# Kernel tuning notes

Hardware: AMD Instinct MI355X
Metric: run time of the kernel (lower is better)

## Reference

```python
import jax, jax.numpy as jnp
from jax import lax
import numpy as np

B, C, H, W = 2, 128, 64, 64
E = 3            # num_experts
DSTATE = 64      # d_state
DCONV = 4        # d_conv
DIN = 2 * C      # d_inner (expand=2)
DTR = 8          # dt_rank = ceil(C/16)
CONVDIM = 64     # router hidden channels


def mamba_block(xseq, in_w, conv_w, conv_b, xproj_w, dt_w, dt_b, A_log, D, out_w):
    # xseq: (B, L, C)
    Bn, L, _ = xseq.shape
    xr = xseq @ in_w.T                      # (B, L, 2*DIN)
    x, res = jnp.split(xr, 2, axis=-1)
    # depthwise causal conv over sequence dim
    xt = x.transpose(0, 2, 1)               # (B, DIN, L)
    xt = lax.conv_general_dilated(xt, conv_w, window_strides=(1,),
                                  padding=[(DCONV - 1, 0)],
                                  feature_group_count=DIN,
                                  dimension_numbers=('NCW', 'OIW', 'NCW'))
    xt = xt + conv_b[None, :, None]
    x = jax.nn.silu(xt.transpose(0, 2, 1))  # (B, L, DIN)
    # input-dependent SSM params
    dbl = x @ xproj_w.T                     # (B, L, DTR + 2*DSTATE)
    dt, Bm, Cm = dbl[..., :DTR], dbl[..., DTR:DTR + DSTATE], dbl[..., DTR + DSTATE:]
    delta = jax.nn.softplus(dt @ dt_w.T + dt_b)  # (B, L, DIN)
    A = -jnp.exp(A_log)                     # (DIN, DSTATE)

    def step(h, inp):
        d_t, B_t, C_t, u_t = inp            # (B,DIN),(B,DSTATE),(B,DSTATE),(B,DIN)
        dA = jnp.exp(d_t[..., None] * A)    # (B, DIN, DSTATE)
        h = dA * h + (d_t * u_t)[..., None] * B_t[:, None, :]
        y = jnp.einsum('bdn,bn->bd', h, C_t)
        return h, y

    h0 = jnp.zeros((Bn, DIN, DSTATE), x.dtype)
    xs = (delta.transpose(1, 0, 2), Bm.transpose(1, 0, 2),
          Cm.transpose(1, 0, 2), x.transpose(1, 0, 2))
    _, ys = lax.scan(step, h0, xs)          # ys: (L, B, DIN)
    y = ys.transpose(1, 0, 2) + x * D       # skip connection
    y = y * jax.nn.silu(res)                # gate
    return y @ out_w.T                      # (B, L, C)


def setup_inputs() -> dict:
    key = jax.random.key(0)
    ks = jax.random.split(key, 10)
    s = 0.02
    n = lambda k, sh: jax.random.normal(k, sh, jnp.float32) * s
    A_log = jnp.log(jnp.broadcast_to(jnp.arange(1, DSTATE + 1, dtype=jnp.float32),
                                     (E, DIN, DSTATE))) + 0.0
    return {
        'x': jax.random.normal(ks[0], (B, C, H, W), jnp.float32),
        'expert_in_w': n(ks[1], (E, 2 * DIN, C)),
        'expert_conv_w': n(ks[2], (E, DIN, 1, DCONV)),
        'expert_conv_b': jnp.zeros((E, DIN), jnp.float32),
        'expert_xproj_w': n(ks[3], (E, DTR + 2 * DSTATE, DIN)),
        'expert_dt_w': n(ks[4], (E, DIN, DTR)),
        'expert_dt_b': jnp.zeros((E, DIN), jnp.float32),
        'expert_A_log': A_log,
        'expert_D': jnp.ones((E, DIN), jnp.float32),
        'expert_out_w': n(ks[5], (E, C, DIN)),
        'router_conv_w': n(ks[6], (CONVDIM, C, 3, 3)),
        'router_conv_b': jnp.zeros((CONVDIM,), jnp.float32),
        'router_lin_w': n(ks[7], (E, CONVDIM)),
        'router_lin_b': jnp.zeros((E,), jnp.float32),
        'fusion_w': n(ks[8], (C, C)),
        'fusion_b': jnp.zeros((C,), jnp.float32),
    }


def reference(x, expert_in_w, expert_conv_w, expert_conv_b, expert_xproj_w,
              expert_dt_w, expert_dt_b, expert_A_log, expert_D, expert_out_w,
              router_conv_w, router_conv_b, router_lin_w, router_lin_b,
              fusion_w, fusion_b):
    Bn, Cn, Hn, Wn = x.shape
    xseq = x.reshape(Bn, Cn, Hn * Wn).transpose(0, 2, 1)  # (B, L, C)
    # router: conv3x3 -> relu -> global avg pool -> linear -> softmax
    r = lax.conv_general_dilated(x, router_conv_w, (1, 1), 'SAME',
                                 dimension_numbers=('NCHW', 'OIHW', 'NCHW'))
    r = jax.nn.relu(r + router_conv_b[None, :, None, None])
    pooled = r.mean(axis=(2, 3))                          # (B, CONVDIM)
    weights = jax.nn.softmax(pooled @ router_lin_w.T + router_lin_b, axis=1)  # (B, E)
    # run all experts via vmap over the expert axis
    outs = jax.vmap(mamba_block, in_axes=(None, 0, 0, 0, 0, 0, 0, 0, 0, 0))(
        xseq, expert_in_w, expert_conv_w, expert_conv_b, expert_xproj_w,
        expert_dt_w, expert_dt_b, expert_A_log, expert_D, expert_out_w)  # (E,B,L,C)
    outs = outs.transpose(0, 1, 3, 2).reshape(outs.shape[0], Bn, Cn, Hn, Wn)
    ws = jnp.einsum('ebchw,be->bchw', outs, weights)
    out = jnp.einsum('bchw,oc->bohw', ws, fusion_w) + fusion_b[None, :, None, None]
    return out
```

## Files before the change

kernel.cpp:

```cpp
#include <hip/hip_runtime.h>
#include <math.h>
#include <stdint.h>

#define LSEQ 4096
#define NCHUNK 8
#define TC 512

#define AS1 __attribute__((address_space(1)))
#define AS3 __attribute__((address_space(3)))
__device__ __forceinline__ void gload_lds16(const void* g, void* l) {
  __builtin_amdgcn_global_load_lds((const AS1 unsigned int*)g,
                                   (AS3 unsigned int*)l, 16, 0, 0);
}

__global__ __launch_bounds__(256) void k_router_conv(
    const float* __restrict__ x, const float* __restrict__ rcw,
    const float* __restrict__ rcb, float* __restrict__ rpool) {
  int bid = blockIdx.x;
  int ocq = bid & 3;
  int h = (bid >> 2) & 63;
  int b = bid >> 8;
  __shared__ float xs[16][3][66];
  __shared__ float wl[16][145];
  int tid = threadIdx.x;
  int ocl = tid & 15;
  int oc = ocq * 16 + ocl;
  int w0 = (tid >> 4) * 4;
  if (tid < 96) {
    int ic = tid / 6, rr = tid % 6;
    int row = rr >> 1, edge = (rr & 1) ? 65 : 0;
    xs[ic][row][edge] = 0.f;
  }
  float acc[4] = {};
  for (int cc = 0; cc < 8; ++cc) {
    __syncthreads();
#pragma unroll
    for (int i = 0; i < 12; ++i) {
      int f = tid + i * 256;
      int ic = f / 192, rem = f % 192;
      int row = rem / 64, w = rem & 63;
      int hh = h - 1 + row;
      float v = 0.f;
      if (hh >= 0 && hh < 64)
        v = x[((size_t)(b * 128 + cc * 16 + ic) * 64 + hh) * 64 + w];
      xs[ic][row][w + 1] = v;
    }
    for (int f = tid; f < 2304; f += 256) {
      int o = f / 144, r = f % 144;
      wl[o][r] = rcw[(size_t)(ocq * 16 + o) * 1152 + cc * 144 + r];
    }
    __syncthreads();
    for (int ic = 0; ic < 16; ++ic) {
#pragma unroll
      for (int kh = 0; kh < 3; ++kh) {
        float xv[6];
#pragma unroll
        for (int j = 0; j < 6; ++j) xv[j] = xs[ic][kh][w0 + j];
        float w_0 = wl[ocl][ic * 9 + kh * 3 + 0];
        float w_1 = wl[ocl][ic * 9 + kh * 3 + 1];
        float w_2 = wl[ocl][ic * 9 + kh * 3 + 2];
#pragma unroll
        for (int i = 0; i < 4; ++i)
          acc[i] += w_0 * xv[i] + w_1 * xv[i + 1] + w_2 * xv[i + 2];
      }
    }
  }
  float cbv = rcb[oc];
  float t = 0.f;
#pragma unroll
  for (int i = 0; i < 4; ++i) t += fmaxf(acc[i] + cbv, 0.f);
  t += __shfl_xor(t, 16);
  t += __shfl_xor(t, 32);
  if ((tid & 63) < 16) atomicAdd(rpool + b * 64 + oc, t);
}

__global__ __launch_bounds__(64) void k_router_softmax(
    const float* __restrict__ rpool, const float* __restrict__ rlw,
    const float* __restrict__ rlb, float* __restrict__ rw) {
  int t = threadIdx.x;
  __shared__ float logits[2][3];
  for (int b = 0; b < 2; ++b) {
    float p = rpool[b * 64 + t] * (1.0f / 4096.0f);
    for (int e = 0; e < 3; ++e) {
      float v = p * rlw[e * 64 + t];
      for (int off = 32; off; off >>= 1) v += __shfl_xor(v, off);
      if (t == 0) logits[b][e] = v + rlb[e];
    }
  }
  __syncthreads();
  if (t == 0) {
    for (int b = 0; b < 2; ++b) {
      float m = fmaxf(fmaxf(logits[b][0], logits[b][1]), logits[b][2]);
      float e0 = expf(logits[b][0] - m), e1 = expf(logits[b][1] - m),
            e2 = expf(logits[b][2] - m);
      float s = e0 + e1 + e2;
      rw[b * 3 + 0] = e0 / s;
      rw[b * 3 + 1] = e1 / s;
      rw[b * 3 + 2] = e2 / s;
    }
  }
}

__global__ __launch_bounds__(256) void k_wfuse(
    const float* __restrict__ fw, const float* __restrict__ outw,
    float* __restrict__ wf) {
  int e = blockIdx.x >> 7;
  int co = blockIdx.x & 127;
  int k = threadIdx.x;
  float acc = 0.f;
  const float* fwr = fw + (size_t)co * 128;
  const float* ob = outw + (size_t)e * 128 * 256 + k;
#pragma unroll 8
  for (int m = 0; m < 128; ++m) acc = fmaf(fwr[m], ob[(size_t)m * 256], acc);
  wf[((size_t)e * 128 + co) * 256 + k] = acc;
}

__global__ __launch_bounds__(256) void k_gemm_in(
    const float* __restrict__ x, const float* __restrict__ inw,
    float* __restrict__ xr) {
  int eb = blockIdx.y;
  int e = eb >> 1, b = eb & 1;
  int lt = blockIdx.x >> 3;
  int jt = blockIdx.x & 7;
  int l0 = lt * 128, j0 = jt * 64;
  __shared__ float xt[16][128];
  __shared__ float wt[16][64];
  int tid = threadIdx.x;
  int jj = (tid & 15) * 4;
  int lr = (tid >> 4) * 8;
  float acc[8][4] = {};
  const float* xb = x + (size_t)b * 128 * 4096;
  const float* wb = inw + (size_t)e * 512 * 128;
  for (int c0 = 0; c0 < 128; c0 += 16) {
    __syncthreads();
#pragma unroll
    for (int i = 0; i < 2; ++i) {
      int f = tid + i * 256;
      int c = f >> 5;
      int lp = (f & 31) * 4;
      float4 v = *(const float4*)(xb + (size_t)(c0 + c) * 4096 + l0 + lp);
      *(float4*)(&xt[c][lp]) = v;
    }
    {
      int j = tid >> 2;
      int kk = (tid & 3) * 4;
      float4 v = *(const float4*)(wb + (size_t)(j0 + j) * 128 + c0 + kk);
      wt[kk + 0][j] = v.x; wt[kk + 1][j] = v.y;
      wt[kk + 2][j] = v.z; wt[kk + 3][j] = v.w;
    }
    __syncthreads();
#pragma unroll
    for (int k = 0; k < 16; ++k) {
      float4 bv = *(const float4*)(&wt[k][jj]);
      float4 a0 = *(const float4*)(&xt[k][lr]);
      float4 a1 = *(const float4*)(&xt[k][lr + 4]);
      float av[8] = {a0.x, a0.y, a0.z, a0.w, a1.x, a1.y, a1.z, a1.w};
#pragma unroll
      for (int i = 0; i < 8; ++i) {
        acc[i][0] = fmaf(av[i], bv.x, acc[i][0]);
        acc[i][1] = fmaf(av[i], bv.y, acc[i][1]);
        acc[i][2] = fmaf(av[i], bv.z, acc[i][2]);
        acc[i][3] = fmaf(av[i], bv.w, acc[i][3]);
      }
    }
  }
  float* out = xr + (size_t)eb * 4096 * 512;
#pragma unroll
  for (int i = 0; i < 8; ++i) {
    float4 v = {acc[i][0], acc[i][1], acc[i][2], acc[i][3]};
    *(float4*)(out + (size_t)(l0 + lr + i) * 512 + j0 + jj) = v;
  }
}

__global__ __launch_bounds__(256) void k_conv1d(
    const float* __restrict__ xr, const float* __restrict__ cw,
    const float* __restrict__ cb, float* __restrict__ xact) {
  int eb = blockIdx.y;
  int e = eb >> 1;
  int l0 = blockIdx.x * 64;
  int d = threadIdx.x;
  const float* w = cw + (size_t)(e * 256 + d) * 4;
  float w0_ = w[0], w1_ = w[1], w2_ = w[2], w3_ = w[3];
  float bias = cb[e * 256 + d];
  const float* xin = xr + (size_t)eb * 4096 * 512 + d;
  float* xo = xact + (size_t)eb * 4096 * 256 + d;
  float xm3 = (l0 >= 3) ? xin[(size_t)(l0 - 3) * 512] : 0.f;
  float xm2 = (l0 >= 2) ? xin[(size_t)(l0 - 2) * 512] : 0.f;
  float xm1 = (l0 >= 1) ? xin[(size_t)(l0 - 1) * 512] : 0.f;
  for (int i = 0; i < 64; ++i) {
    float xc = xin[(size_t)(l0 + i) * 512];
    float v = bias + w0_ * xm3 + w1_ * xm2 + w2_ * xm1 + w3_ * xc;
    xo[(size_t)(l0 + i) * 256] = v / (1.0f + expf(-v));
    xm3 = xm2; xm2 = xm1; xm1 = xc;
  }
}

__global__ __launch_bounds__(256) void k_gemm_xproj(
    const float* __restrict__ xact, const float* __restrict__ xpw,
    float* __restrict__ dbl) {
  int eb = blockIdx.y;
  int e = eb >> 1;
  int lt = blockIdx.x / 3, jt = blockIdx.x % 3;
  int l0 = lt * 128, j0 = jt * 64;
  __shared__ float at[16][128];
  __shared__ float wt[16][64];
  int tid = threadIdx.x;
  int jj = (tid & 15) * 4;
  int lr = (tid >> 4) * 8;
  float acc[8][4] = {};
  const float* ab = xact + (size_t)eb * 4096 * 256;
  const float* wb = xpw + (size_t)e * 136 * 256;
  for (int k0 = 0; k0 < 256; k0 += 16) {
    __syncthreads();
#pragma unroll
    for (int i = 0; i < 2; ++i) {
      int f = tid + i * 256;
      int l = f >> 2, kq = (f & 3) * 4;
      float4 v = *(const float4*)(ab + (size_t)(l0 + l) * 256 + k0 + kq);
      at[kq + 0][l] = v.x; at[kq + 1][l] = v.y;
      at[kq + 2][l] = v.z; at[kq + 3][l] = v.w;
    }
    {
      int j = tid >> 2, kk = (tid & 3) * 4;
      float4 v = {0, 0, 0, 0};
      if (j0 + j < 136)
        v = *(const float4*)(wb + (size_t)(j0 + j) * 256 + k0 + kk);
      wt[kk + 0][j] = v.x; wt[kk + 1][j] = v.y;
      wt[kk + 2][j] = v.z; wt[kk + 3][j] = v.w;
    }
    __syncthreads();
#pragma unroll
    for (int k = 0; k < 16; ++k) {
      float4 bv = *(const float4*)(&wt[k][jj]);
      float4 a0 = *(const float4*)(&at[k][lr]);
      float4 a1 = *(const float4*)(&at[k][lr + 4]);
      float av[8] = {a0.x, a0.y, a0.z, a0.w, a1.x, a1.y, a1.z, a1.w};
#pragma unroll
      for (int i = 0; i < 8; ++i) {
        acc[i][0] = fmaf(av[i], bv.x, acc[i][0]);
        acc[i][1] = fmaf(av[i], bv.y, acc[i][1]);
        acc[i][2] = fmaf(av[i], bv.z, acc[i][2]);
        acc[i][3] = fmaf(av[i], bv.w, acc[i][3]);
      }
    }
  }
  float* ob = dbl + (size_t)eb * 4096 * 136;
  for (int i = 0; i < 8; ++i)
    for (int q = 0; q < 4; ++q) {
      int j = j0 + jj + q;
      if (j < 136) ob[(size_t)(l0 + lr + i) * 136 + j] = acc[i][q];
    }
}

__global__ __launch_bounds__(256) void k_delta(
    const float* __restrict__ dbl, const float* __restrict__ dtw,
    const float* __restrict__ dtb, const float* __restrict__ xact,
    float* __restrict__ dd) {
  int eb = blockIdx.y;
  int e = eb >> 1;
  int t0 = blockIdx.x * 64;
  int d = threadIdx.x;
  __shared__ float dt8[64][8];
  {
    int f = threadIdx.x;
    for (int i = 0; i < 2; ++i, f += 256) {
      int l = f >> 3, r = f & 7;
      dt8[l][r] = dbl[(size_t)eb * 4096 * 136 + (size_t)(t0 + l) * 136 + r];
    }
  }
  __syncthreads();
  float w[8];
#pragma unroll
  for (int r = 0; r < 8; ++r) w[r] = dtw[(size_t)(e * 256 + d) * 8 + r];
  float bias = dtb[e * 256 + d];
  const float* xa = xact + (size_t)eb * 4096 * 256 + d;
  float4* out = (float4*)dd + (size_t)(eb * 256 + d) * 2048 + (t0 >> 1);
  for (int i = 0; i < 64; i += 2) {
    float v0 = bias, v1 = bias;
#pragma unroll
    for (int r = 0; r < 8; ++r) {
      v0 += dt8[i][r] * w[r];
      v1 += dt8[i + 1][r] * w[r];
    }
    float de0 = fmaxf(v0, 0.f) + log1pf(expf(-fabsf(v0)));
    float de1 = fmaxf(v1, 0.f) + log1pf(expf(-fabsf(v1)));
    float u0 = xa[(size_t)(t0 + i) * 256];
    float u1 = xa[(size_t)(t0 + i + 1) * 256];
    float4 o = {de0, de0 * u0, de1, de1 * u1};
    out[i >> 1] = o;
  }
}

__global__ __launch_bounds__(256) void k_scan1(
    const float* __restrict__ dbl, const float* __restrict__ dd,
    const float* __restrict__ alog, float* __restrict__ prd,
    float* __restrict__ hend) {
  __shared__ float sB[2][16][64];
  int eb = blockIdx.y;
  int e = eb >> 1;
  int c = blockIdx.x >> 6;
  int dgrp = blockIdx.x & 63;
  int wid = threadIdx.x >> 6, lane = threadIdx.x & 63;
  int d = dgrp * 4 + wid;
  float An = -__expf(alog[((size_t)e * 256 + d) * 64 + lane]);
  const float2* ddp = (const float2*)dd + ((size_t)eb * 256 + d) * 4096;
  {
    uint64_t a = (uint64_t)ddp;
    uint32_t lo = __builtin_amdgcn_readfirstlane((int)(uint32_t)a);
    uint32_t hi = __builtin_amdgcn_readfirstlane((int)(uint32_t)(a >> 32));
    ddp = (const float2*)(((uint64_t)hi << 32) | (uint64_t)lo);
  }
  const float* dblb = dbl + (size_t)eb * 4096 * 136;
  int t0 = c * TC;
  int srow = 4 * wid + (lane >> 4);
  int scol = (lane & 15) * 4;
  float h = 0.f, sdel = 0.f;
  gload_lds16(dblb + (size_t)(t0 + srow) * 136 + 8 + scol, &sB[0][4 * wid][0]);
  __syncthreads();
  for (int s = 0; s < 32; ++s) {
    int cur = s & 1;
    int t0s = t0 + s * 16;
    if (s + 1 < 32)
      gload_lds16(dblb + (size_t)(t0s + 16 + srow) * 136 + 8 + scol,
                  &sB[cur ^ 1][4 * wid][0]);
    float2 rdv[16];
#pragma unroll
    for (int j = 0; j < 16; ++j) rdv[j] = ddp[t0s + j];
#pragma unroll
    for (int j = 0; j < 16; ++j) {
      float Bn = sB[cur][j][lane];
      h = fmaf(__expf(rdv[j].x * An), h, rdv[j].y * Bn);
      sdel += rdv[j].x;
    }
    __syncthreads();
  }
  size_t o = (((size_t)eb * 256 + d) * NCHUNK + c) * 64 + lane;
  prd[o] = __expf(An * sdel);
  hend[o] = h;
}

__global__ __launch_bounds__(256) void k_scan2(
    const float* __restrict__ prd, const float* __restrict__ hend,
    float* __restrict__ hinit) {
  int w = blockIdx.x * 4 + (threadIdx.x >> 6);
  int lane = threadIdx.x & 63;
  size_t base = (size_t)w * NCHUNK * 64 + lane;
  float h = 0.f;
  hinit[base] = 0.f;
#pragma unroll
  for (int c = 1; c < NCHUNK; ++c) {
    h = fmaf(prd[base + (c - 1) * 64], h, hend[base + (c - 1) * 64]);
    hinit[base + c * 64] = h;
  }
}

__global__ __launch_bounds__(256) void k_scan3(
    const float* __restrict__ dbl, const float* __restrict__ dd,
    const float* __restrict__ alog, const float* __restrict__ hinit,
    float* __restrict__ ytr) {
  __shared__ float sBC[2][16][128];
  __shared__ float P[4][16][65];
  int eb = blockIdx.y;
  int e = eb >> 1;
  int c = blockIdx.x >> 6;
  int dgrp = blockIdx.x & 63;
  int wid = threadIdx.x >> 6, lane = threadIdx.x & 63;
  int d = dgrp * 4 + wid;
  float An = -__expf(alog[((size_t)e * 256 + d) * 64 + lane]);
  const float2* ddp = (const float2*)dd + ((size_t)eb * 256 + d) * 4096;
  {
    uint64_t a = (uint64_t)ddp;
    uint32_t lo = __builtin_amdgcn_readfirstlane((int)(uint32_t)a);
    uint32_t hi = __builtin_amdgcn_readfirstlane((int)(uint32_t)(a >> 32));
    ddp = (const float2*)(((uint64_t)hi << 32) | (uint64_t)lo);
  }
  const float* dblb = dbl + (size_t)eb * 4096 * 136;
  int t0 = c * TC;
  int scol = (lane & 31) * 4;
  int srow0 = 4 * wid + (lane >> 5);
  float h = hinit[(((size_t)eb * 256 + d) * NCHUNK + c) * 64 + lane];
  float* yout = ytr + ((size_t)eb * 256 + d) * 4096;
  int r = lane & 15, q = lane >> 4;
  gload_lds16(dblb + (size_t)(t0 + srow0) * 136 + 8 + scol, &sBC[0][4 * wid][0]);
  gload_lds16(dblb + (size_t)(t0 + srow0 + 2) * 136 + 8 + scol,
              &sBC[0][4 * wid + 2][0]);
  __syncthreads();
  for (int s = 0; s < 32; ++s) {
    int cur = s & 1;
    int t0s = t0 + s * 16;
    if (s + 1 < 32) {
      gload_lds16(dblb + (size_t)(t0s + 16 + srow0) * 136 + 8 + scol,
                  &sBC[cur ^ 1][4 * wid][0]);
      gload_lds16(dblb + (size_t)(t0s + 16 + srow0 + 2) * 136 + 8 + scol,
                  &sBC[cur ^ 1][4 * wid + 2][0]);
    }
    float2 rdv[16];
#pragma unroll
    for (int j = 0; j < 16; ++j) rdv[j] = ddp[t0s + j];
#pragma unroll
    for (int j = 0; j < 16; ++j) {
      float Bn = sBC[cur][j][lane];
      float Cn = sBC[cur][j][64 + lane];
      h = fmaf(__expf(rdv[j].x * An), h, rdv[j].y * Bn);
      P[wid][j][lane] = h * Cn;
    }
    float acc = 0.f;
#pragma unroll
    for (int k = 0; k < 16; ++k) acc += P[wid][r][q * 16 + k];
    acc += __shfl_xor(acc, 16);
    acc += __shfl_xor(acc, 32);
    if (q == 0) yout[t0s + r] = acc;
    __syncthreads();
  }
}

__global__ __launch_bounds__(256) void k_yfuse(
    const float* __restrict__ ytr, const float* __restrict__ xact,
    const float* __restrict__ xr, const float* __restrict__ Dw,
    float* __restrict__ yf) {
  int eb = blockIdx.y;
  int e = eb >> 1;
  int dti = blockIdx.x >> 6, tti = blockIdx.x & 63;
  int d0 = dti * 64, t0 = tti * 64;
  __shared__ float sp[64][65];
  __shared__ float sq[64][65];
  int tid = threadIdx.x;
  int j = tid & 63;
  int r0 = tid >> 6;
  float Dj = Dw[e * 256 + d0 + j];
  const float* xab = xact + (size_t)eb * 4096 * 256;
  const float* xrb = xr + (size_t)eb * 4096 * 512;
#pragma unroll
  for (int it = 0; it < 16; ++it) {
    int r = r0 + it * 4;
    float xa = xab[(size_t)(t0 + r) * 256 + d0 + j];
    float rs = xrb[(size_t)(t0 + r) * 512 + 256 + d0 + j];
    float pch = rs / (1.0f + expf(-rs));
    sp[r][j] = pch;
    sq[r][j] = xa * Dj * pch;
  }
  __syncthreads();
#pragma unroll
  for (int it = 0; it < 16; ++it) {
    int ddr = r0 + it * 4;
    size_t idx = ((size_t)eb * 256 + d0 + ddr) * 4096 + t0 + j;
    float y = ytr[idx];
    yf[idx] = y * sp[j][ddr] + sq[j][ddr];
  }
}

__global__ __launch_bounds__(256) void k_gemm_out2(
    const float* __restrict__ yf, const float* __restrict__ wf,
    const float* __restrict__ rw, const float* __restrict__ fb,
    float* __restrict__ out) {
  int b = blockIdx.y;
  int tt = blockIdx.x >> 1;
  int ct = blockIdx.x & 1;
  int t0 = tt * 64, c0 = ct * 64;
  __shared__ float at[16][66];
  __shared__ float wt[16][64];
  int tid = threadIdx.x;
  int co4 = (tid & 15) * 4;
  int t4 = (tid >> 4) * 4;
  float acc[4][4] = {};
  for (int e = 0; e < 3; ++e) {
    float wbe = rw[b * 3 + e];
    const float* ab = yf + (size_t)(e * 2 + b) * 256 * 4096;
    const float* wb = wf + (size_t)e * 128 * 256;
    for (int k0 = 0; k0 < 256; k0 += 16) {
      __syncthreads();
      {
#pragma unroll
        for (int i = 0; i < 4; ++i) {
          int f = tid + i * 256;
          int t = f & 63, k = f >> 6;
          at[k][t] = ab[(size_t)(k0 + k) * 4096 + t0 + t];
        }
        int jc = tid >> 2, kk = (tid & 3) * 4;
        float4 v = *(const float4*)(wb + (size_t)(c0 + jc) * 256 + k0 + kk);
        wt[kk + 0][jc] = v.x * wbe; wt[kk + 1][jc] = v.y * wbe;
        wt[kk + 2][jc] = v.z * wbe; wt[kk + 3][jc] = v.w * wbe;
      }
      __syncthreads();
#pragma unroll
      for (int k = 0; k < 16; ++k) {
        float4 bv = *(const float4*)(&wt[k][co4]);
        float4 av = *(const float4*)(&at[k][t4]);
        float a_[4] = {av.x, av.y, av.z, av.w};
#pragma unroll
        for (int i = 0; i < 4; ++i) {
          acc[i][0] = fmaf(a_[i], bv.x, acc[i][0]);
          acc[i][1] = fmaf(a_[i], bv.y, acc[i][1]);
          acc[i][2] = fmaf(a_[i], bv.z, acc[i][2]);
          acc[i][3] = fmaf(a_[i], bv.w, acc[i][3]);
        }
      }
    }
  }
#pragma unroll
  for (int o = 0; o < 4; ++o) {
    float bias = fb[c0 + co4 + o];
    float4 v = {acc[0][o] + bias, acc[1][o] + bias, acc[2][o] + bias,
                acc[3][o] + bias};
    *(float4*)(out + ((size_t)(b * 128 + c0 + co4 + o)) * 4096 + t0 + t4) = v;
  }
}

extern "C" void kernel_launch(void* const* d_in, const int* in_sizes, int n_in,
                              void* d_out, int out_size, void* d_ws,
                              size_t ws_size, hipStream_t stream) {
  const float* x    = (const float*)d_in[0];
  const float* inw  = (const float*)d_in[1];
  const float* cw   = (const float*)d_in[2];
  const float* cb   = (const float*)d_in[3];
  const float* xpw  = (const float*)d_in[4];
  const float* dtw  = (const float*)d_in[5];
  const float* dtb  = (const float*)d_in[6];
  const float* alog = (const float*)d_in[7];
  const float* Dw   = (const float*)d_in[8];
  const float* outw = (const float*)d_in[9];
  const float* rcw  = (const float*)d_in[10];
  const float* rcb  = (const float*)d_in[11];
  const float* rlw  = (const float*)d_in[12];
  const float* rlb  = (const float*)d_in[13];
  const float* fw   = (const float*)d_in[14];
  const float* fb   = (const float*)d_in[15];

  float* ws = (float*)d_ws;
  float* XR    = ws;
  float* XACT  = ws + 12582912;
  float* DBL   = ws + 18874368;
  float* DD    = ws + 22216704;
  float* YTR   = ws + 34799616;
  float* MIX   = ws + 41091072;
  float* RPOOL = ws + 42139648;
  float* RW    = ws + 42139776;
  float* YF    = DD;
  float* PRD   = YTR;
  float* HEND  = YTR + 786432;
  float* HINIT = MIX;
  float* WF    = MIX + 786432;

  if (ws_size < (size_t)42139784 * sizeof(float)) return;

  hipMemsetAsync(RPOOL, 0, 128 * sizeof(float), stream);
  k_router_conv<<<512, 256, 0, stream>>>(x, rcw, rcb, RPOOL);
  k_router_softmax<<<1, 64, 0, stream>>>(RPOOL, rlw, rlb, RW);
  k_wfuse<<<384, 256, 0, stream>>>(fw, outw, WF);
  k_gemm_in<<<dim3(256, 6), 256, 0, stream>>>(x, inw, XR);
  k_conv1d<<<dim3(64, 6), 256, 0, stream>>>(XR, cw, cb, XACT);
  k_gemm_xproj<<<dim3(96, 6), 256, 0, stream>>>(XACT, xpw, DBL);
  k_delta<<<dim3(64, 6), 256, 0, stream>>>(DBL, dtw, dtb, XACT, DD);
  k_scan1<<<dim3(64 * 7, 6), 256, 0, stream>>>(DBL, DD, alog, PRD, HEND);
  k_scan2<<<384, 256, 0, stream>>>(PRD, HEND, HINIT);
  k_scan3<<<dim3(64 * NCHUNK, 6), 256, 0, stream>>>(DBL, DD, alog, HINIT, YTR);
  k_yfuse<<<dim3(256, 6), 256, 0, stream>>>(YTR, XACT, XR, Dw, YF);
  k_gemm_out2<<<dim3(128, 2), 256, 0, stream>>>(YF, WF, RW, fb, (float*)d_out);
}
```

Before: 582.8 us.

## Process two channels per wave in scans and replace LDS reduction with shuffle transpose

Each wave in the chunked scan kernels now handles two d_inner channels instead of one. This halves the block count and reuses each LDS-staged B/C row for both channels, which also gives two independent recurrence chains for latency hiding. In scan3, the per-step LDS scratch array and its 16-way reduction are replaced by a butterfly shuffle-based transpose-reduce (reduce16) with bit-reversed output indexing. The trade-offs are higher register pressure, fewer blocks in flight, and extra shuffle instructions.

```diff
diff --git a/kernel.cpp b/kernel.cpp
--- a/kernel.cpp
+++ b/kernel.cpp
@@ -11,6 +11,40 @@
 __device__ __forceinline__ void gload_lds16(const void* g, void* l) {
   __builtin_amdgcn_global_load_lds((const AS1 unsigned int*)g,
                                    (AS3 unsigned int*)l, 16, 0, 0);
+}
+
+__device__ __forceinline__ float reduce16(const float* p, int lane) {
+  float q[8];
+  int s0 = lane & 1;
+#pragma unroll
+  for (int j = 0; j < 8; ++j) {
+    float send = s0 ? p[j] : p[j + 8];
+    float keep = s0 ? p[j + 8] : p[j];
+    q[j] = keep + __shfl_xor(send, 1);
+  }
+  float r_[4];
+  int s1 = (lane >> 1) & 1;
+#pragma unroll
+  for (int j = 0; j < 4; ++j) {
+    float send = s1 ? q[j] : q[j + 4];
+    float keep = s1 ? q[j + 4] : q[j];
+    r_[j] = keep + __shfl_xor(send, 2);
+  }
+  float t_[2];
+  int s2 = (lane >> 2) & 1;
+#pragma unroll
+  for (int j = 0; j < 2; ++j) {
+    float send = s2 ? t_[0] * 0.f + r_[j] : r_[j + 2];
+    float keep = s2 ? r_[j + 2] : r_[j];
+    t_[j] = keep + __shfl_xor(send, 4);
+  }
+  int s3 = (lane >> 3) & 1;
+  float send = s3 ? t_[0] : t_[1];
+  float keep = s3 ? t_[1] : t_[0];
+  float u = keep + __shfl_xor(send, 8);
+  u += __shfl_xor(u, 16);
+  u += __shfl_xor(u, 32);
+  return u;
 }
 
 __global__ __launch_bounds__(256) void k_router_conv(
@@ -298,23 +332,26 @@
   __shared__ float sB[2][16][64];
   int eb = blockIdx.y;
   int e = eb >> 1;
-  int c = blockIdx.x >> 6;
-  int dgrp = blockIdx.x & 63;
+  int c = blockIdx.x >> 5;
+  int dgrp = blockIdx.x & 31;
   int wid = threadIdx.x >> 6, lane = threadIdx.x & 63;
-  int d = dgrp * 4 + wid;
-  float An = -__expf(alog[((size_t)e * 256 + d) * 64 + lane]);
-  const float2* ddp = (const float2*)dd + ((size_t)eb * 256 + d) * 4096;
+  int d0 = dgrp * 8 + wid * 2;
+  float An0 = -__expf(alog[((size_t)e * 256 + d0) * 64 + lane]);
+  float An1 = -__expf(alog[((size_t)e * 256 + d0 + 1) * 64 + lane]);
+  const float2* ddp0 = (const float2*)dd + ((size_t)eb * 256 + d0) * 4096;
+  const float2* ddp1 = ddp0 + 4096;
   {
-    uint64_t a = (uint64_t)ddp;
+    uint64_t a = (uint64_t)ddp0;
     uint32_t lo = __builtin_amdgcn_readfirstlane((int)(uint32_t)a);
     uint32_t hi = __builtin_amdgcn_readfirstlane((int)(uint32_t)(a >> 32));
-    ddp = (const float2*)(((uint64_t)hi << 32) | (uint64_t)lo);
+    ddp0 = (const float2*)(((uint64_t)hi << 32) | (uint64_t)lo);
+    ddp1 = ddp0 + 4096;
   }
   const float* dblb = dbl + (size_t)eb * 4096 * 136;
   int t0 = c * TC;
   int srow = 4 * wid + (lane >> 4);
   int scol = (lane & 15) * 4;
-  float h = 0.f, sdel = 0.f;
+  float h0 = 0.f, h1 = 0.f, sd0 = 0.f, sd1 = 0.f;
   gload_lds16(dblb + (size_t)(t0 + srow) * 136 + 8 + scol, &sB[0][4 * wid][0]);
   __syncthreads();
   for (int s = 0; s < 32; ++s) {
@@ -323,20 +360,24 @@
     if (s + 1 < 32)
       gload_lds16(dblb + (size_t)(t0s + 16 + srow) * 136 + 8 + scol,
                   &sB[cur ^ 1][4 * wid][0]);
-    float2 rdv[16];
-#pragma unroll
-    for (int j = 0; j < 16; ++j) rdv[j] = ddp[t0s + j];
 #pragma unroll
     for (int j = 0; j < 16; ++j) {
+      float2 dv0 = ddp0[t0s + j];
+      float2 dv1 = ddp1[t0s + j];
       float Bn = sB[cur][j][lane];
-      h = fmaf(__expf(rdv[j].x * An), h, rdv[j].y * Bn);
-      sdel += rdv[j].x;
-    }
-    __syncthreads();
-  }
-  size_t o = (((size_t)eb * 256 + d) * NCHUNK + c) * 64 + lane;
-  prd[o] = __expf(An * sdel);
-  hend[o] = h;
+      h0 = fmaf(__expf(dv0.x * An0), h0, dv0.y * Bn);
+      h1 = fmaf(__expf(dv1.x * An1), h1, dv1.y * Bn);
+      sd0 += dv0.x;
+      sd1 += dv1.x;
+    }
+    __syncthreads();
+  }
+  size_t o0 = (((size_t)eb * 256 + d0) * NCHUNK + c) * 64 + lane;
+  prd[o0] = __expf(An0 * sd0);
+  hend[o0] = h0;
+  size_t o1 = o0 + (size_t)NCHUNK * 64;
+  prd[o1] = __expf(An1 * sd1);
+  hend[o1] = h1;
 }
 
 __global__ __launch_bounds__(256) void k_scan2(
@@ -359,28 +400,33 @@
     const float* __restrict__ alog, const float* __restrict__ hinit,
     float* __restrict__ ytr) {
   __shared__ float sBC[2][16][128];
-  __shared__ float P[4][16][65];
   int eb = blockIdx.y;
   int e = eb >> 1;
-  int c = blockIdx.x >> 6;
-  int dgrp = blockIdx.x & 63;
+  int c = blockIdx.x >> 5;
+  int dgrp = blockIdx.x & 31;
   int wid = threadIdx.x >> 6, lane = threadIdx.x & 63;
-  int d = dgrp * 4 + wid;
-  float An = -__expf(alog[((size_t)e * 256 + d) * 64 + lane]);
-  const float2* ddp = (const float2*)dd + ((size_t)eb * 256 + d) * 4096;
+  int d0 = dgrp * 8 + wid * 2;
+  float An0 = -__expf(alog[((size_t)e * 256 + d0) * 64 + lane]);
+  float An1 = -__expf(alog[((size_t)e * 256 + d0 + 1) * 64 + lane]);
+  const float2* ddp0 = (const float2*)dd + ((size_t)eb * 256 + d0) * 4096;
+  const float2* ddp1 = ddp0 + 4096;
   {
-    uint64_t a = (uint64_t)ddp;
+    uint64_t a = (uint64_t)ddp0;
     uint32_t lo = __builtin_amdgcn_readfirstlane((int)(uint32_t)a);
     uint32_t hi = __builtin_amdgcn_readfirstlane((int)(uint32_t)(a >> 32));
-    ddp = (const float2*)(((uint64_t)hi << 32) | (uint64_t)lo);
+    ddp0 = (const float2*)(((uint64_t)hi << 32) | (uint64_t)lo);
+    ddp1 = ddp0 + 4096;
   }
   const float* dblb = dbl + (size_t)eb * 4096 * 136;
   int t0 = c * TC;
   int scol = (lane & 31) * 4;
   int srow0 = 4 * wid + (lane >> 5);
-  float h = hinit[(((size_t)eb * 256 + d) * NCHUNK + c) * 64 + lane];
-  float* yout = ytr + ((size_t)eb * 256 + d) * 4096;
-  int r = lane & 15, q = lane >> 4;
+  float h0 = hinit[(((size_t)eb * 256 + d0) * NCHUNK + c) * 64 + lane];
+  float h1 = hinit[(((size_t)eb * 256 + d0 + 1) * NCHUNK + c) * 64 + lane];
+  float* yout0 = ytr + ((size_t)eb * 256 + d0) * 4096;
+  float* yout1 = yout0 + 4096;
+  int toff = ((lane & 1) << 3) | (((lane >> 1) & 1) << 2) |
+             (((lane >> 2) & 1) << 1) | ((lane >> 3) & 1);
   gload_lds16(dblb + (size_t)(t0 + srow0) * 136 + 8 + scol, &sBC[0][4 * wid][0]);
   gload_lds16(dblb + (size_t)(t0 + srow0 + 2) * 136 + 8 + scol,
               &sBC[0][4 * wid + 2][0]);
@@ -394,22 +440,24 @@
       gload_lds16(dblb + (size_t)(t0s + 16 + srow0 + 2) * 136 + 8 + scol,
                   &sBC[cur ^ 1][4 * wid + 2][0]);
     }
-    float2 rdv[16];
-#pragma unroll
-    for (int j = 0; j < 16; ++j) rdv[j] = ddp[t0s + j];
+    float p0[16], p1[16];
 #pragma unroll
     for (int j = 0; j < 16; ++j) {
+      float2 dv0 = ddp0[t0s + j];
+      float2 dv1 = ddp1[t0s + j];
       float Bn = sBC[cur][j][lane];
       float Cn = sBC[cur][j][64 + lane];
-      h = fmaf(__expf(rdv[j].x * An), h, rdv[j].y * Bn);
-      P[wid][j][lane] = h * Cn;
-    }
-    float acc = 0.f;
-#pragma unroll
-    for (int k = 0; k < 16; ++k) acc += P[wid][r][q * 16 + k];
-    acc += __shfl_xor(acc, 16);
-    acc += __shfl_xor(acc, 32);
-    if (q == 0) yout[t0s + r] = acc;
+      h0 = fmaf(__expf(dv0.x * An0), h0, dv0.y * Bn);
+      h1 = fmaf(__expf(dv1.x * An1), h1, dv1.y * Bn);
+      p0[j] = h0 * Cn;
+      p1[j] = h1 * Cn;
+    }
+    float y0 = reduce16(p0, lane);
+    float y1 = reduce16(p1, lane);
+    if (lane < 16) {
+      yout0[t0s + toff] = y0;
+      yout1[t0s + toff] = y1;
+    }
     __syncthreads();
   }
 }
@@ -551,9 +599,9 @@
   k_conv1d<<<dim3(64, 6), 256, 0, stream>>>(XR, cw, cb, XACT);
   k_gemm_xproj<<<dim3(96, 6), 256, 0, stream>>>(XACT, xpw, DBL);
   k_delta<<<dim3(64, 6), 256, 0, stream>>>(DBL, dtw, dtb, XACT, DD);
-  k_scan1<<<dim3(64 * 7, 6), 256, 0, stream>>>(DBL, DD, alog, PRD, HEND);
+  k_scan1<<<dim3(32 * 7, 6), 256, 0, stream>>>(DBL, DD, alog, PRD, HEND);
   k_scan2<<<384, 256, 0, stream>>>(PRD, HEND, HINIT);
-  k_scan3<<<dim3(64 * NCHUNK, 6), 256, 0, stream>>>(DBL, DD, alog, HINIT, YTR);
+  k_scan3<<<dim3(32 * NCHUNK, 6), 256, 0, stream>>>(DBL, DD, alog, HINIT, YTR);
   k_yfuse<<<dim3(256, 6), 256, 0, stream>>>(YTR, XACT, XR, Dw, YF);
   k_gemm_out2<<<dim3(128, 2), 256, 0, stream>>>(YF, WF, RW, fb, (float*)d_out);
 }
```

Result: slower. 642.4 us (+10.2%).

## Process two channels per wave in chunked scans with shuffle-based C reduction

Applied to the files above, without the earlier changes.

Each wave in the chunked selective-scan kernels now handles two d_inner channels instead of one. This gives two independent recurrences to interleave, reuses each B/C LDS read twice, and loads the delta stream as float4. Scan3 replaces its LDS staging buffer and reduction over 16 timesteps with a register butterfly transpose-reduce over 8 timesteps using shuffles. The exponentials use exp2f with a prescaled A. In exchange the grid is halved and register pressure rises, which the new launch bounds try to limit.

```diff
diff --git a/kernel.cpp b/kernel.cpp
--- a/kernel.cpp
+++ b/kernel.cpp
@@ -291,52 +291,100 @@
   }
 }
 
-__global__ __launch_bounds__(256) void k_scan1(
+#define CRED8(P, U)                                   \
+  {                                                   \
+    float qq_[4];                                     \
+    int s0_ = lane & 1;                               \
+    _Pragma("unroll") for (int j_ = 0; j_ < 4; ++j_) {\
+      float se_ = s0_ ? P[j_] : P[j_ + 4];            \
+      float ke_ = s0_ ? P[j_ + 4] : P[j_];            \
+      qq_[j_] = ke_ + __shfl_xor(se_, 1);             \
+    }                                                 \
+    float rr_[2];                                     \
+    int s1_ = (lane >> 1) & 1;                        \
+    _Pragma("unroll") for (int j_ = 0; j_ < 2; ++j_) {\
+      float se_ = s1_ ? qq_[j_] : qq_[j_ + 2];        \
+      float ke_ = s1_ ? qq_[j_ + 2] : qq_[j_];        \
+      rr_[j_] = ke_ + __shfl_xor(se_, 2);             \
+    }                                                 \
+    int s2_ = (lane >> 2) & 1;                        \
+    float se_ = s2_ ? rr_[0] : rr_[1];                \
+    float ke_ = s2_ ? rr_[1] : rr_[0];                \
+    U = ke_ + __shfl_xor(se_, 4);                     \
+    U += __shfl_xor(U, 8);                            \
+    U += __shfl_xor(U, 16);                           \
+    U += __shfl_xor(U, 32);                           \
+  }
+
+#define S1T2(QAX, QAY, QBX, QBY, ROW)                 \
+  {                                                   \
+    float Bn = sB[cur][ROW][lane];                    \
+    h0 = fmaf(exp2f((QAX)*An20), h0, (QAY)*Bn);       \
+    sd0 += (QAX);                                     \
+    h1 = fmaf(exp2f((QBX)*An21), h1, (QBY)*Bn);       \
+    sd1 += (QBX);                                     \
+  }
+
+__global__ __launch_bounds__(256, 8) void k_scan1(
     const float* __restrict__ dbl, const float* __restrict__ dd,
     const float* __restrict__ alog, float* __restrict__ prd,
     float* __restrict__ hend) {
   __shared__ float sB[2][16][64];
   int eb = blockIdx.y;
   int e = eb >> 1;
-  int c = blockIdx.x >> 6;
-  int dgrp = blockIdx.x & 63;
+  int c = blockIdx.x >> 5;
+  int dgrp = blockIdx.x & 31;
   int wid = threadIdx.x >> 6, lane = threadIdx.x & 63;
-  int d = dgrp * 4 + wid;
-  float An = -__expf(alog[((size_t)e * 256 + d) * 64 + lane]);
-  const float2* ddp = (const float2*)dd + ((size_t)eb * 256 + d) * 4096;
+  int d0 = dgrp * 8 + wid * 2;
+  float An20 = -__expf(alog[((size_t)e * 256 + d0) * 64 + lane]) * 1.44269504f;
+  float An21 =
+      -__expf(alog[((size_t)e * 256 + d0 + 1) * 64 + lane]) * 1.44269504f;
+  const float2* ddp = (const float2*)dd + ((size_t)eb * 256 + d0) * 4096;
   {
     uint64_t a = (uint64_t)ddp;
     uint32_t lo = __builtin_amdgcn_readfirstlane((int)(uint32_t)a);
     uint32_t hi = __builtin_amdgcn_readfirstlane((int)(uint32_t)(a >> 32));
     ddp = (const float2*)(((uint64_t)hi << 32) | (uint64_t)lo);
   }
+  const float4* dq0 = (const float4*)ddp;
+  const float4* dq1 = dq0 + 2048;
   const float* dblb = dbl + (size_t)eb * 4096 * 136;
   int t0 = c * TC;
   int srow = 4 * wid + (lane >> 4);
   int scol = (lane & 15) * 4;
-  float h = 0.f, sdel = 0.f;
+  float h0 = 0.f, h1 = 0.f, sd0 = 0.f, sd1 = 0.f;
   gload_lds16(dblb + (size_t)(t0 + srow) * 136 + 8 + scol, &sB[0][4 * wid][0]);
   __syncthreads();
-  for (int s = 0; s < 32; ++s) {
-    int cur = s & 1;
-    int t0s = t0 + s * 16;
-    if (s + 1 < 32)
-      gload_lds16(dblb + (size_t)(t0s + 16 + srow) * 136 + 8 + scol,
+  for (int sb = 0; sb < 32; ++sb) {
+    int cur = sb & 1;
+    if (sb + 1 < 32)
+      gload_lds16(dblb + (size_t)(t0 + (sb + 1) * 16 + srow) * 136 + 8 + scol,
                   &sB[cur ^ 1][4 * wid][0]);
-    float2 rdv[16];
-#pragma unroll
-    for (int j = 0; j < 16; ++j) rdv[j] = ddp[t0s + j];
-#pragma unroll
-    for (int j = 0; j < 16; ++j) {
-      float Bn = sB[cur][j][lane];
-      h = fmaf(__expf(rdv[j].x * An), h, rdv[j].y * Bn);
-      sdel += rdv[j].x;
-    }
-    __syncthreads();
-  }
-  size_t o = (((size_t)eb * 256 + d) * NCHUNK + c) * 64 + lane;
-  prd[o] = __expf(An * sdel);
-  hend[o] = h;
+#pragma unroll
+    for (int g = 0; g < 2; ++g) {
+      int qA = (t0 >> 1) + sb * 8 + g * 4;
+      float4 a0 = dq0[qA + 0], a1 = dq0[qA + 1], a2 = dq0[qA + 2],
+             a3 = dq0[qA + 3];
+      float4 b0 = dq1[qA + 0], b1 = dq1[qA + 1], b2 = dq1[qA + 2],
+             b3 = dq1[qA + 3];
+      int R = g * 8;
+      S1T2(a0.x, a0.y, b0.x, b0.y, R + 0)
+      S1T2(a0.z, a0.w, b0.z, b0.w, R + 1)
+      S1T2(a1.x, a1.y, b1.x, b1.y, R + 2)
+      S1T2(a1.z, a1.w, b1.z, b1.w, R + 3)
+      S1T2(a2.x, a2.y, b2.x, b2.y, R + 4)
+      S1T2(a2.z, a2.w, b2.z, b2.w, R + 5)
+      S1T2(a3.x, a3.y, b3.x, b3.y, R + 6)
+      S1T2(a3.z, a3.w, b3.z, b3.w, R + 7)
+    }
+    __syncthreads();
+  }
+  size_t o0 = (((size_t)eb * 256 + d0) * NCHUNK + c) * 64 + lane;
+  prd[o0] = exp2f(An20 * sd0);
+  hend[o0] = h0;
+  size_t o1 = o0 + (size_t)NCHUNK * 64;
+  prd[o1] = exp2f(An21 * sd1);
+  hend[o1] = h1;
 }
 
 __global__ __launch_bounds__(256) void k_scan2(
@@ -354,62 +402,88 @@
   }
 }
 
-__global__ __launch_bounds__(256) void k_scan3(
+#define S3T2(QAX, QAY, QBX, QBY, ROW, J)              \
+  {                                                   \
+    float Bn = sBC[cur][ROW][lane];                   \
+    float Cn = sBC[cur][ROW][64 + lane];              \
+    h0 = fmaf(exp2f((QAX)*An20), h0, (QAY)*Bn);       \
+    p0[J] = h0 * Cn;                                  \
+    h1 = fmaf(exp2f((QBX)*An21), h1, (QBY)*Bn);       \
+    p1[J] = h1 * Cn;                                  \
+  }
+
+__global__ __launch_bounds__(256, 6) void k_scan3(
     const float* __restrict__ dbl, const float* __restrict__ dd,
     const float* __restrict__ alog, const float* __restrict__ hinit,
     float* __restrict__ ytr) {
   __shared__ float sBC[2][16][128];
-  __shared__ float P[4][16][65];
   int eb = blockIdx.y;
   int e = eb >> 1;
-  int c = blockIdx.x >> 6;
-  int dgrp = blockIdx.x & 63;
+  int c = blockIdx.x >> 5;
+  int dgrp = blockIdx.x & 31;
   int wid = threadIdx.x >> 6, lane = threadIdx.x & 63;
-  int d = dgrp * 4 + wid;
-  float An = -__expf(alog[((size_t)e * 256 + d) * 64 + lane]);
-  const float2* ddp = (const float2*)dd + ((size_t)eb * 256 + d) * 4096;
+  int d0 = dgrp * 8 + wid * 2;
+  float An20 = -__expf(alog[((size_t)e * 256 + d0) * 64 + lane]) * 1.44269504f;
+  float An21 =
+      -__expf(alog[((size_t)e * 256 + d0 + 1) * 64 + lane]) * 1.44269504f;
+  const float2* ddp = (const float2*)dd + ((size_t)eb * 256 + d0) * 4096;
   {
     uint64_t a = (uint64_t)ddp;
     uint32_t lo = __builtin_amdgcn_readfirstlane((int)(uint32_t)a);
     uint32_t hi = __builtin_amdgcn_readfirstlane((int)(uint32_t)(a >> 32));
     ddp = (const float2*)(((uint64_t)hi << 32) | (uint64_t)lo);
   }
+  const float4* dq0 = (const float4*)ddp;
+  const float4* dq1 = dq0 + 2048;
   const float* dblb = dbl + (size_t)eb * 4096 * 136;
   int t0 = c * TC;
   int scol = (lane & 31) * 4;
   int srow0 = 4 * wid + (lane >> 5);
-  float h = hinit[(((size_t)eb * 256 + d) * NCHUNK + c) * 64 + lane];
-  float* yout = ytr + ((size_t)eb * 256 + d) * 4096;
-  int r = lane & 15, q = lane >> 4;
-  gload_lds16(dblb + (size_t)(t0 + srow0) * 136 + 8 + scol, &sBC[0][4 * wid][0]);
+  float h0 = hinit[(((size_t)eb * 256 + d0) * NCHUNK + c) * 64 + lane];
+  float h1 = hinit[(((size_t)eb * 256 + d0 + 1) * NCHUNK + c) * 64 + lane];
+  float* yout0 = ytr + ((size_t)eb * 256 + d0) * 4096;
+  float* yout1 = yout0 + 4096;
+  int toff = ((lane & 1) << 2) | (lane & 2) | ((lane >> 2) & 1);
+  gload_lds16(dblb + (size_t)(t0 + srow0) * 136 + 8 + scol,
+              &sBC[0][4 * wid][0]);
   gload_lds16(dblb + (size_t)(t0 + srow0 + 2) * 136 + 8 + scol,
               &sBC[0][4 * wid + 2][0]);
   __syncthreads();
-  for (int s = 0; s < 32; ++s) {
-    int cur = s & 1;
-    int t0s = t0 + s * 16;
-    if (s + 1 < 32) {
-      gload_lds16(dblb + (size_t)(t0s + 16 + srow0) * 136 + 8 + scol,
+  for (int sb = 0; sb < 32; ++sb) {
+    int cur = sb & 1;
+    if (sb + 1 < 32) {
+      int tN = t0 + (sb + 1) * 16;
+      gload_lds16(dblb + (size_t)(tN + srow0) * 136 + 8 + scol,
                   &sBC[cur ^ 1][4 * wid][0]);
-      gload_lds16(dblb + (size_t)(t0s + 16 + srow0 + 2) * 136 + 8 + scol,
+      gload_lds16(dblb + (size_t)(tN + srow0 + 2) * 136 + 8 + scol,
                   &sBC[cur ^ 1][4 * wid + 2][0]);
     }
-    float2 rdv[16];
-#pragma unroll
-    for (int j = 0; j < 16; ++j) rdv[j] = ddp[t0s + j];
-#pragma unroll
-    for (int j = 0; j < 16; ++j) {
-      float Bn = sBC[cur][j][lane];
-      float Cn = sBC[cur][j][64 + lane];
-      h = fmaf(__expf(rdv[j].x * An), h, rdv[j].y * Bn);
-      P[wid][j][lane] = h * Cn;
-    }
-    float acc = 0.f;
-#pragma unroll
-    for (int k = 0; k < 16; ++k) acc += P[wid][r][q * 16 + k];
-    acc += __shfl_xor(acc, 16);
-    acc += __shfl_xor(acc, 32);
-    if (q == 0) yout[t0s + r] = acc;
+#pragma unroll
+    for (int g = 0; g < 2; ++g) {
+      int tA = t0 + sb * 16 + g * 8;
+      int qA = tA >> 1;
+      float4 a0 = dq0[qA + 0], a1 = dq0[qA + 1], a2 = dq0[qA + 2],
+             a3 = dq0[qA + 3];
+      float4 b0 = dq1[qA + 0], b1 = dq1[qA + 1], b2 = dq1[qA + 2],
+             b3 = dq1[qA + 3];
+      float p0[8], p1[8];
+      int R = g * 8;
+      S3T2(a0.x, a0.y, b0.x, b0.y, R + 0, 0)
+      S3T2(a0.z, a0.w, b0.z, b0.w, R + 1, 1)
+      S3T2(a1.x, a1.y, b1.x, b1.y, R + 2, 2)
+      S3T2(a1.z, a1.w, b1.z, b1.w, R + 3, 3)
+      S3T2(a2.x, a2.y, b2.x, b2.y, R + 4, 4)
+      S3T2(a2.z, a2.w, b2.z, b2.w, R + 5, 5)
+      S3T2(a3.x, a3.y, b3.x, b3.y, R + 6, 6)
+      S3T2(a3.z, a3.w, b3.z, b3.w, R + 7, 7)
+      float u0, u1;
+      CRED8(p0, u0)
+      CRED8(p1, u1)
+      if (lane < 8) {
+        yout0[tA + toff] = u0;
+        yout1[tA + toff] = u1;
+      }
+    }
     __syncthreads();
   }
 }
@@ -551,9 +625,9 @@
   k_conv1d<<<dim3(64, 6), 256, 0, stream>>>(XR, cw, cb, XACT);
   k_gemm_xproj<<<dim3(96, 6), 256, 0, stream>>>(XACT, xpw, DBL);
   k_delta<<<dim3(64, 6), 256, 0, stream>>>(DBL, dtw, dtb, XACT, DD);
-  k_scan1<<<dim3(64 * 7, 6), 256, 0, stream>>>(DBL, DD, alog, PRD, HEND);
+  k_scan1<<<dim3(32 * 7, 6), 256, 0, stream>>>(DBL, DD, alog, PRD, HEND);
   k_scan2<<<384, 256, 0, stream>>>(PRD, HEND, HINIT);
-  k_scan3<<<dim3(64 * NCHUNK, 6), 256, 0, stream>>>(DBL, DD, alog, HINIT, YTR);
+  k_scan3<<<dim3(32 * NCHUNK, 6), 256, 0, stream>>>(DBL, DD, alog, HINIT, YTR);
   k_yfuse<<<dim3(256, 6), 256, 0, stream>>>(YTR, XACT, XR, Dw, YF);
   k_gemm_out2<<<dim3(128, 2), 256, 0, stream>>>(YF, WF, RW, fb, (float*)d_out);
 }
```

Result: slower. 873.3 us (+49.9%).
